# Optimization experiments

Hardware: AMD Instinct MI355X
Metric: run time of the kernel (lower is better)

## Reference

```python
import jax, jax.numpy as jnp
import numpy as np

L = 3          # num encoder layers
H = 128        # hidden_dim
NH = 8         # num_heads
HD = H // NH   # head_dim
FF = H * 4     # ff inner dim (after GLU)
B, N = 32, 512
NUM_BINS = 50


def _linear_params(key, fan_in, fan_out):
    kw, kb = jax.random.split(key)
    lim = 1.0 / np.sqrt(fan_in)
    W = jax.random.uniform(kw, (fan_in, fan_out), jnp.float32, -lim, lim)
    b = jax.random.uniform(kb, (fan_out,), jnp.float32, -lim, lim)
    return W, b


def setup_inputs() -> dict:
    key = jax.random.key(0)
    ks = jax.random.split(key, 16)
    x = jax.random.normal(ks[0], (B, N, H), jnp.float32)
    distance_matrix = jax.random.uniform(ks[1], (B, N, N), jnp.float32)
    mask = jax.random.randint(ks[2], (B, N), 0, 2).astype(bool)

    def stack_linear(k, fan_in, fan_out):
        Ws, bs = [], []
        for l in range(L):
            W, b = _linear_params(jax.random.fold_in(k, l), fan_in, fan_out)
            Ws.append(W); bs.append(b)
        return jnp.stack(Ws), jnp.stack(bs)

    Wq, bq = stack_linear(ks[3], H, H)
    Wk, bk = stack_linear(ks[4], H, H)
    Wv, bv = stack_linear(ks[5], H, H)
    Wo, bo = stack_linear(ks[6], H, H)
    dist_emb = jax.random.normal(ks[7], (L, NUM_BINS, NH), jnp.float32)
    attn_bias = jnp.zeros((L, NH, 1, 1), jnp.float32)
    g1 = jnp.ones((L, H), jnp.float32); b1 = jnp.zeros((L, H), jnp.float32)
    g2 = jnp.ones((L, H), jnp.float32); b2 = jnp.zeros((L, H), jnp.float32)
    Wf1, bf1 = stack_linear(ks[8], H, 2 * FF)
    Wf2, bf2 = stack_linear(ks[9], FF, H)
    return dict(x=x, distance_matrix=distance_matrix, mask=mask,
                Wq=Wq, bq=bq, Wk=Wk, bk=bk, Wv=Wv, bv=bv, Wo=Wo, bo=bo,
                dist_emb=dist_emb, attn_bias=attn_bias,
                g1=g1, b1=b1, g2=g2, b2=b2,
                Wf1=Wf1, bf1=bf1, Wf2=Wf2, bf2=bf2)


def _layernorm(x, g, b, eps=1e-5):
    mu = jnp.mean(x, axis=-1, keepdims=True)
    var = jnp.var(x, axis=-1, keepdims=True)
    return (x - mu) * jax.lax.rsqrt(var + eps) * g + b


def _attention(h, bins, key_mask, Wq, bq, Wk, bk, Wv, bv, Wo, bo, dist_emb, attn_bias):
    # h: [B,N,H]; bins: [B,N,N] int; key_mask: [B,N] bool (True = masked)
    Bsz, Nn, _ = h.shape
    Q = (h @ Wq + bq).reshape(Bsz, Nn, NH, HD)
    K = (h @ Wk + bk).reshape(Bsz, Nn, NH, HD)
    V = (h @ Wv + bv).reshape(Bsz, Nn, NH, HD)
    scores = jnp.einsum('bqhd,bkhd->bhqk', Q, K) / np.sqrt(HD)
    bias = jnp.transpose(dist_emb[bins], (0, 3, 1, 2))  # [B,NH,N,N]
    scores = scores + bias + attn_bias[None]
    scores = jnp.where(key_mask[:, None, None, :], -1e9, scores)
    attn = jax.nn.softmax(scores, axis=-1)
    out = jnp.einsum('bhqk,bkhd->bqhd', attn, V).reshape(Bsz, Nn, H)
    return out @ Wo + bo


def reference(x, distance_matrix, mask, Wq, bq, Wk, bk, Wv, bv, Wo, bo,
              dist_emb, attn_bias, g1, b1, g2, b2, Wf1, bf1, Wf2, bf2):
    bins = jnp.clip((distance_matrix * 10.0).astype(jnp.int32), 0, NUM_BINS - 1)
    h = x
    for l in range(L):
        # pre-LN attention block
        a = _attention(_layernorm(h, g1[l], b1[l]), bins, mask,
                       Wq[l], bq[l], Wk[l], bk[l], Wv[l], bv[l], Wo[l], bo[l],
                       dist_emb[l], attn_bias[l])
        h = h + a
        # pre-LN GLU feed-forward
        u = _layernorm(h, g2[l], b2[l]) @ Wf1[l] + bf1[l]  # [B,N,2*FF]
        ua, ub = jnp.split(u, 2, axis=-1)
        h = h + (ua * jax.nn.sigmoid(ub)) @ Wf2[l] + bf2[l]
    return h
```

## Files before the change

### kernel.cpp

```cpp
#include <hip/hip_runtime.h>
#include <stdint.h>

#define Bq 32
#define Nq 512
#define Hq 128
#define NHq 8
#define HDq 16
#define Mq (Bq * Nq)

typedef unsigned short u16;
typedef __attribute__((ext_vector_type(8))) short short8;
typedef __attribute__((ext_vector_type(8))) _Float16 half8;
typedef __attribute__((ext_vector_type(2))) __fp16 fp16x2;
typedef __attribute__((ext_vector_type(4))) float f32x4;

__device__ __forceinline__ float bf2f(u16 v) {
    return __uint_as_float(((unsigned int)v) << 16);
}
__device__ __forceinline__ float ldin(const void* p, long idx, int bf) {
    if (bf) return bf2f(((const u16*)p)[idx]);
    return ((const float*)p)[idx];
}
__device__ __forceinline__ u16 f2bf(float v) {
    unsigned int u = __float_as_uint(v);
    return (u16)((u + 0x7FFFu + ((u >> 16) & 1u)) >> 16);
}
__device__ __forceinline__ u16 f2h(float v) {
    _Float16 h = (_Float16)v;
    return *(u16*)&h;
}
__device__ __forceinline__ unsigned pk2h(float a, float b) {
    fp16x2 c = __builtin_amdgcn_cvt_pkrtz(a, b);
    return *(unsigned*)&c;
}

__global__ void prep_kernel(const void* xraw, const void* de, const void* ab,
                            const void* mraw, int* flag, float* deo, float* abo,
                            unsigned* mbits, int n) {
    __shared__ int cnt, orA, orB, orC, orD;
    int tid = threadIdx.x;
    if (tid == 0) { cnt = 0; orA = 0; orB = 0; orC = 0; orD = 0; }
    __syncthreads();
    const u16* u = (const u16*)xraw;
    int good = 0;
    for (int i = tid; i < 1024; i += 256) {
        u16 v = u[i];
        int e = (v >> 7) & 0xFF;
        if (v == 0 || (e >= 90 && e <= 141)) good++;
    }
    atomicAdd(&cnt, good);
    const uint4* p4 = (const uint4*)mraw;
    unsigned a = 0, b = 0, c = 0, d = 0;
    for (int i = tid; i < n / 16; i += 256) {
        uint4 w = p4[i];
        unsigned all = w.x | w.y | w.z | w.w;
        a |= all & 0xFEFEFEFEu;
        b |= all & 0x0000FF00u;
        c |= all & 0xFFFFFF00u;
        d |= w.y | w.w;
    }
    if (a) atomicOr(&orA, 1);
    if (b) atomicOr(&orB, 1);
    if (c) atomicOr(&orC, 1);
    if (d) atomicOr(&orD, 1);
    __syncthreads();
    int bf = (cnt >= 900);
    if (tid == 0) *flag = bf;
    int mode;
    if (orA) mode = orB ? 3 : 4;
    else if (orC) mode = 0;
    else mode = orD ? 1 : 2;
    for (int i = tid; i < 1200; i += 256) deo[i] = ldin(de, i, bf);
    if (tid < 24) abo[tid] = ldin(ab, tid, bf);
    const unsigned char* p = (const unsigned char*)mraw;
    for (int wI = tid; wI < n / 32; wI += 256) {
        unsigned word = 0;
        for (int j = 0; j < 32; ++j) {
            int i = wI * 32 + j;
            int v;
            switch (mode) {
                case 0: v = p[i]; break;
                case 1: v = ((const int*)p)[i]; break;
                case 2: v = (int)((const long long*)p)[i]; break;
                case 3: v = ((const u16*)p)[i] != 0; break;
                default: v = (((const float*)p)[i] != 0.0f); break;
            }
            if (v) word |= 1u << j;
        }
        mbits[wI] = word;
    }
}

__global__ void kprep_kernel(const unsigned* __restrict__ mbits,
                             u16* __restrict__ kidxg, int* __restrict__ nkt,
                             unsigned* __restrict__ tmask) {
    int b = blockIdx.x;
    int lane = threadIdx.x & 63;
    int pos_base = 0;
    for (int w = 0; w < 8; ++w) {
        unsigned lo = mbits[b * 16 + 2 * w], hi = mbits[b * 16 + 2 * w + 1];
        unsigned long long word = ((unsigned long long)hi << 32) | lo;
        unsigned long long un = ~word;
        int bit = (int)((un >> lane) & 1ull);
        unsigned long long before = un & ((1ull << lane) - 1ull);
        int pos = pos_base + __popcll(before);
        if (bit) kidxg[b * 512 + pos] = (u16)(w * 64 + lane);
        pos_base += __popcll(un);
    }
    int nk = pos_base;
    int nkp = (nk + 31) & ~31;
    if (nkp == 0) nkp = 32;
    int nt = nkp >> 5;
    for (int j = nk + lane; j < nkp; j += 64) kidxg[b * 512 + j] = 0;
    if (lane == 0) {
        nkt[b] = nt;
        for (int t = 0; t < 16; ++t) tmask[b * 16 + t] = 0;
        int rem = nk & 31;
        if (rem) tmask[b * 16 + nt - 1] = 0xFFFFFFFFu << rem;
        if (nk == 0) tmask[b * 16] = 0xFFFFFFFFu;
    }
}

__global__ __launch_bounds__(256) void binsc_kernel(
    const void* __restrict__ dist, const u16* __restrict__ kidxg,
    const int* __restrict__ nkt, unsigned char* __restrict__ binsc,
    const int* flagp) {
    int bf = *flagp;
    int b = blockIdx.y;
    int q0 = blockIdx.x * 8;
    __shared__ u16 kl[512];
    __shared__ int ntS;
    int tid = threadIdx.x;
    if (tid == 0) ntS = nkt[b];
    kl[tid] = kidxg[b * 512 + tid];
    kl[tid + 256] = kidxg[b * 512 + tid + 256];
    __syncthreads();
    int nkp = ntS * 32;
    for (int rq = 0; rq < 8; ++rq) {
        int q = q0 + rq;
        long rowoff = ((long)b * 512 + q) * 512;
        for (int j = tid; j < nkp; j += 256) {
            float d = ldin(dist, rowoff + kl[j], bf);
            int v = (int)(d * 10.0f);
            v = v < 0 ? 0 : (v > 49 ? 49 : v);
            binsc[((size_t)b * 512 + q) * 512 + j] = (unsigned char)(v << 2);
        }
    }
}

__global__ __launch_bounds__(256) void init_kernel(const void* x,
                                                   float* __restrict__ h,
                                                   const int* flagp) {
    int bf = *flagp;
    int i = blockIdx.x * 256 + threadIdx.x;
    long base = (long)i * 8;
    if (bf) {
        uint4 w = ((const uint4*)x)[i];
        const u16* ws = (const u16*)&w;
        float o[8];
#pragma unroll
        for (int k = 0; k < 8; ++k) o[k] = bf2f(ws[k]);
        *(float4*)&h[base] = *(float4*)&o[0];
        *(float4*)&h[base + 4] = *(float4*)&o[4];
    } else {
        float4 a = ((const float4*)x)[2 * i];
        float4 b = ((const float4*)x)[2 * i + 1];
        *(float4*)&h[base] = a;
        *(float4*)&h[base + 4] = b;
    }
}

__global__ __launch_bounds__(256) void wtrans_kernel(
    const void* Wqr, const void* Wkr, const void* Wvr, const void* Wor,
    const void* Wf1r, const void* Wf2r,
    u16* qkvT, u16* oT, u16* f1T, u16* f2T, const int* flagp) {
    int bf = *flagp;
    int bid = blockIdx.x;
    int l = bid >> 8, r = bid & 255;
    const void* src; u16* dst; long soff, doff; int Kd, Nd, t;
    if (r < 64) {
        int mat = r >> 4; t = r & 15; Kd = 128; Nd = 128;
        soff = (long)l * 16384;
        if (mat == 0)      { src = Wqr; dst = qkvT; doff = (long)l * 49152; }
        else if (mat == 1) { src = Wkr; dst = qkvT; doff = (long)l * 49152 + 16384; }
        else if (mat == 2) { src = Wvr; dst = qkvT; doff = (long)l * 49152 + 32768; }
        else               { src = Wor; dst = oT;   doff = (long)l * 16384; }
    } else if (r < 192) {
        t = r - 64; Kd = 128; Nd = 1024;
        src = Wf1r; soff = (long)l * 131072; dst = f1T; doff = (long)l * 131072;
    } else {
        t = r - 192; Kd = 512; Nd = 128;
        src = Wf2r; soff = (long)l * 65536; dst = f2T; doff = (long)l * 65536;
    }
    int ntile = Nd >> 5;
    int tk = t / ntile, tn = t % ntile;
    __shared__ u16 Ts[32][33];
    int rr = threadIdx.x >> 3, cc0 = (threadIdx.x & 7) * 4;
#pragma unroll
    for (int i = 0; i < 4; ++i) {
        long idx = soff + (long)(tk * 32 + rr) * Nd + tn * 32 + cc0 + i;
        Ts[rr][cc0 + i] = f2bf(ldin(src, idx, bf));
    }
    __syncthreads();
#pragma unroll
    for (int i = 0; i < 4; ++i) {
        long idx = doff + (long)(tn * 32 + rr) * Kd + tk * 32 + cc0 + i;
        dst[idx] = Ts[cc0 + i][rr];
    }
}

__global__ __launch_bounds__(256, 4) void qkv_mfma_kernel(
    const float* __restrict__ h, const u16* __restrict__ qkvT_l,
    const void* bqr, const void* bkr, const void* bvr, long bOff,
    const void* g1raw, const void* b1raw, long lnOff,
    u16* __restrict__ Qo, u16* __restrict__ Ko, u16* __restrict__ Vo,
    const int* flagp) {
    __shared__ __align__(16) u16 As[32][136];
    int tid = threadIdx.x;
    int m0 = blockIdx.x * 32;
    int bf = *flagp;
    {
        int row = tid >> 3, c0 = (tid & 7) * 16;
        const float* hp = h + (size_t)(m0 + row) * 128 + c0;
        float4 f0 = *(const float4*)(hp);
        float4 f1 = *(const float4*)(hp + 4);
        float4 f2 = *(const float4*)(hp + 8);
        float4 f3 = *(const float4*)(hp + 12);
        float vv[16] = {f0.x, f0.y, f0.z, f0.w, f1.x, f1.y, f1.z, f1.w,
                        f2.x, f2.y, f2.z, f2.w, f3.x, f3.y, f3.z, f3.w};
        float s = 0.f, s2 = 0.f;
#pragma unroll
        for (int k = 0; k < 16; ++k) { s += vv[k]; s2 += vv[k] * vv[k]; }
#pragma unroll
        for (int o = 1; o < 8; o <<= 1) {
            s += __shfl_xor(s, o);
            s2 += __shfl_xor(s2, o);
        }
        float mu = s * (1.0f / 128.0f);
        float var = fmaxf(s2 * (1.0f / 128.0f) - mu * mu, 0.0f);
        float rstd = rsqrtf(var + 1e-5f);
        u16 tmp[16];
#pragma unroll
        for (int k = 0; k < 16; ++k) {
            float g = ldin(g1raw, lnOff + c0 + k, bf);
            float b = ldin(b1raw, lnOff + c0 + k, bf);
            tmp[k] = f2bf((vv[k] - mu) * rstd * g + b);
        }
        *(uint4*)&As[row][c0]     = *(uint4*)&tmp[0];
        *(uint4*)&As[row][c0 + 8] = *(uint4*)&tmp[8];
    }
    __syncthreads();
    int wave = tid >> 6, lane = tid & 63;
    int q = lane >> 4, ln = lane & 15;
    int nb = wave * 32;
    f32x4 zero = {0.f, 0.f, 0.f, 0.f};
#pragma unroll
    for (int mat = 0; mat < 3; ++mat) {
        const u16* WT = qkvT_l + (size_t)mat * 16384;
        const void* braw = mat == 0 ? bqr : (mat == 1 ? bkr : bvr);
        u16* C = mat == 0 ? Qo : (mat == 1 ? Ko : Vo);
        float scale = mat == 0 ? 0.25f : 1.0f;
        short8 bfr[2][4];
#pragma unroll
        for (int t = 0; t < 2; ++t)
#pragma unroll
            for (int k4 = 0; k4 < 4; ++k4)
                bfr[t][k4] = *(const short8*)(WT + (size_t)(nb + t * 16 + ln) * 128
                                              + k4 * 32 + q * 8);
        f32x4 acc[2][2];
#pragma unroll
        for (int i = 0; i < 2; ++i)
#pragma unroll
            for (int j = 0; j < 2; ++j) acc[i][j] = zero;
#pragma unroll
        for (int k4 = 0; k4 < 4; ++k4) {
            short8 af0 = *(const short8*)&As[ln][k4 * 32 + q * 8];
            short8 af1 = *(const short8*)&As[16 + ln][k4 * 32 + q * 8];
#pragma unroll
            for (int t = 0; t < 2; ++t) {
                acc[0][t] = __builtin_amdgcn_mfma_f32_16x16x32_bf16(
                    af0, bfr[t][k4], acc[0][t], 0, 0, 0);
                acc[1][t] = __builtin_amdgcn_mfma_f32_16x16x32_bf16(
                    af1, bfr[t][k4], acc[1][t], 0, 0, 0);
            }
        }
#pragma unroll
        for (int t = 0; t < 2; ++t) {
            int n = nb + t * 16 + ln;
            float bias = ldin(braw, bOff + n, bf);
#pragma unroll
            for (int mi = 0; mi < 2; ++mi)
#pragma unroll
                for (int r = 0; r < 4; ++r) {
                    int m = m0 + mi * 16 + q * 4 + r;
                    C[(size_t)m * 128 + n] = f2h((acc[mi][t][r] + bias) * scale);
                }
        }
    }
}

__global__ __launch_bounds__(256, 3) void ffglu_kernel(
    const u16* __restrict__ att, const u16* __restrict__ oT_l,
    const void* __restrict__ bo, long boOff, float* __restrict__ h,
    const void* g2, const void* b2, long ln2Off,
    const u16* __restrict__ f1T_l, const void* __restrict__ bf1r, long bf1Off,
    const u16* __restrict__ f2T_l, const void* __restrict__ bf2r, long bf2Off,
    void* __restrict__ outp, const int* flagp) {
    __shared__ __align__(16) u16 As[32][136];
    __shared__ __align__(16) u16 vg[32][520];
    __shared__ float stats[32][4][2];
    int tid = threadIdx.x;
    int m0 = blockIdx.x * 32;
    int wave = tid >> 6, lane = tid & 63;
    int q = lane >> 4, ln = lane & 15;
    int nb = wave * 32;
    int bf = *flagp;
    f32x4 zero = {0.f, 0.f, 0.f, 0.f};

#pragma unroll
    for (int i = 0; i < 2; ++i) {
        int idx = tid + i * 256; int r = idx >> 4, c = (idx & 15) << 3;
        *(uint4*)&As[r][c] = *(const uint4*)(att + (size_t)(m0 + r) * 128 + c);
    }
    __syncthreads();
    f32x4 acc[2][2];
#pragma unroll
    for (int i = 0; i < 2; ++i)
#pragma unroll
        for (int j = 0; j < 2; ++j) acc[i][j] = zero;
    {
        short8 bfr[2][4];
#pragma unroll
        for (int t = 0; t < 2; ++t)
#pragma unroll
            for (int k4 = 0; k4 < 4; ++k4)
                bfr[t][k4] = *(const short8*)(oT_l + (size_t)(nb + t * 16 + ln) * 128
                                              + k4 * 32 + q * 8);
#pragma unroll
        for (int k4 = 0; k4 < 4; ++k4) {
            short8 af0 = *(const short8*)&As[ln][k4 * 32 + q * 8];
            short8 af1 = *(const short8*)&As[16 + ln][k4 * 32 + q * 8];
#pragma unroll
            for (int t = 0; t < 2; ++t) {
                acc[0][t] = __builtin_amdgcn_mfma_f32_16x16x32_bf16(
                    af0, bfr[t][k4], acc[0][t], 0, 0, 0);
                acc[1][t] = __builtin_amdgcn_mfma_f32_16x16x32_bf16(
                    af1, bfr[t][k4], acc[1][t], 0, 0, 0);
            }
        }
    }
    float h1[2][2][4];
    float srow[2][4], s2row[2][4];
#pragma unroll
    for (int mi = 0; mi < 2; ++mi)
#pragma unroll
        for (int r = 0; r < 4; ++r) { srow[mi][r] = 0.f; s2row[mi][r] = 0.f; }
#pragma unroll
    for (int t = 0; t < 2; ++t) {
        int n = nb + t * 16 + ln;
        float bias = ldin(bo, boOff + n, bf);
#pragma unroll
        for (int mi = 0; mi < 2; ++mi)
#pragma unroll
            for (int r = 0; r < 4; ++r) {
                float v = acc[mi][t][r] + bias +
                          h[(size_t)(m0 + mi * 16 + q * 4 + r) * 128 + n];
                h1[mi][t][r] = v;
                srow[mi][r] += v; s2row[mi][r] += v * v;
            }
    }
#pragma unroll
    for (int mi = 0; mi < 2; ++mi)
#pragma unroll
        for (int r = 0; r < 4; ++r)
#pragma unroll
            for (int o = 1; o < 16; o <<= 1) {
                srow[mi][r] += __shfl_xor(srow[mi][r], o);
                s2row[mi][r] += __shfl_xor(s2row[mi][r], o);
            }
    if (ln == 0) {
#pragma unroll
        for (int mi = 0; mi < 2; ++mi)
#pragma unroll
            for (int r = 0; r < 4; ++r) {
                stats[mi * 16 + q * 4 + r][wave][0] = srow[mi][r];
                stats[mi * 16 + q * 4 + r][wave][1] = s2row[mi][r];
            }
    }
    __syncthreads();
    float mu[2][4], rs[2][4];
#pragma unroll
    for (int mi = 0; mi < 2; ++mi)
#pragma unroll
        for (int r = 0; r < 4; ++r) {
            int row = mi * 16 + q * 4 + r;
            float s = (stats[row][0][0] + stats[row][1][0]) +
                      (stats[row][2][0] + stats[row][3][0]);
            float s2 = (stats[row][0][1] + stats[row][1][1]) +
                       (stats[row][2][1] + stats[row][3][1]);
            mu[mi][r] = s * (1.0f / 128.0f);
            float var = fmaxf(s2 * (1.0f / 128.0f) - mu[mi][r] * mu[mi][r], 0.0f);
            rs[mi][r] = rsqrtf(var + 1e-5f);
        }
#pragma unroll
    for (int t = 0; t < 2; ++t) {
        int n = nb + t * 16 + ln;
        float g = ldin(g2, ln2Off + n, bf), bb = ldin(b2, ln2Off + n, bf);
#pragma unroll
        for (int mi = 0; mi < 2; ++mi)
#pragma unroll
            for (int r = 0; r < 4; ++r)
                As[mi * 16 + q * 4 + r][n] =
                    f2bf((h1[mi][t][r] - mu[mi][r]) * rs[mi][r] * g + bb);
    }
    __syncthreads();
    int nb16 = wave * 16;
    for (int ch = 0; ch < 8; ++ch) {
        int arow = ch * 64 + nb16;
        short8 ba[4], bb8[4];
#pragma unroll
        for (int k4 = 0; k4 < 4; ++k4) {
            ba[k4]  = *(const short8*)(f1T_l + (size_t)(arow + ln) * 128
                                       + k4 * 32 + q * 8);
            bb8[k4] = *(const short8*)(f1T_l + (size_t)(512 + arow + ln) * 128
                                       + k4 * 32 + q * 8);
        }
        f32x4 aA[2] = {zero, zero}, aB[2] = {zero, zero};
#pragma unroll
        for (int k4 = 0; k4 < 4; ++k4) {
            short8 af0 = *(const short8*)&As[ln][k4 * 32 + q * 8];
            short8 af1 = *(const short8*)&As[16 + ln][k4 * 32 + q * 8];
            aA[0] = __builtin_amdgcn_mfma_f32_16x16x32_bf16(af0, ba[k4], aA[0], 0, 0, 0);
            aA[1] = __builtin_amdgcn_mfma_f32_16x16x32_bf16(af1, ba[k4], aA[1], 0, 0, 0);
            aB[0] = __builtin_amdgcn_mfma_f32_16x16x32_bf16(af0, bb8[k4], aB[0], 0, 0, 0);
            aB[1] = __builtin_amdgcn_mfma_f32_16x16x32_bf16(af1, bb8[k4], aB[1], 0, 0, 0);
        }
        int n = arow + ln;
        float bA = ldin(bf1r, bf1Off + n, bf);
        float bB = ldin(bf1r, bf1Off + 512 + n, bf);
#pragma unroll
        for (int mi = 0; mi < 2; ++mi)
#pragma unroll
            for (int r = 0; r < 4; ++r) {
                float ua = aA[mi][r] + bA, ub = aB[mi][r] + bB;
                vg[mi * 16 + q * 4 + r][n] = f2bf(ua / (1.0f + __expf(-ub)));
            }
    }
    __syncthreads();
    f32x4 accF[2][2];
#pragma unroll
    for (int i = 0; i < 2; ++i)
#pragma unroll
        for (int j = 0; j < 2; ++j) accF[i][j] = zero;
    for (int fc = 0; fc < 4; ++fc) {
        short8 bfr[2][4];
#pragma unroll
        for (int t = 0; t < 2; ++t)
#pragma unroll
            for (int k4 = 0; k4 < 4; ++k4)
                bfr[t][k4] = *(const short8*)(f2T_l + (size_t)(nb + t * 16 + ln) * 512
                                              + fc * 128 + k4 * 32 + q * 8);
#pragma unroll
        for (int k4 = 0; k4 < 4; ++k4) {
            short8 af0 = *(const short8*)&vg[ln][fc * 128 + k4 * 32 + q * 8];
            short8 af1 = *(const short8*)&vg[16 + ln][fc * 128 + k4 * 32 + q * 8];
#pragma unroll
            for (int t = 0; t < 2; ++t) {
                accF[0][t] = __builtin_amdgcn_mfma_f32_16x16x32_bf16(
                    af0, bfr[t][k4], accF[0][t], 0, 0, 0);
                accF[1][t] = __builtin_amdgcn_mfma_f32_16x16x32_bf16(
                    af1, bfr[t][k4], accF[1][t], 0, 0, 0);
            }
        }
    }
#pragma unroll
    for (int t = 0; t < 2; ++t) {
        int n = nb + t * 16 + ln;
        float bias = ldin(bf2r, bf2Off + n, bf);
#pragma unroll
        for (int mi = 0; mi < 2; ++mi)
#pragma unroll
            for (int r = 0; r < 4; ++r) {
                int m = m0 + mi * 16 + q * 4 + r;
                float v = accF[mi][t][r] + bias + h1[mi][t][r];
                h[(size_t)m * 128 + n] = v;
                if (outp) {
                    if (bf) ((u16*)outp)[(size_t)m * 128 + n] = f2bf(v);
                    else ((float*)outp)[(size_t)m * 128 + n] = v;
                }
            }
    }
}

__global__ __launch_bounds__(256, 4) void attn_kernel(
    const u16* __restrict__ Qh, const u16* __restrict__ Kh,
    const u16* __restrict__ Vh, const unsigned char* __restrict__ binsc,
    const u16* __restrict__ kidxg, const int* __restrict__ nktp,
    const unsigned* __restrict__ tmaskp, const float* __restrict__ deL,
    const float* __restrict__ abL, u16* __restrict__ out) {
    int id = blockIdx.x;
    int c = id & 7, t5 = id >> 3;
    int nh = t5 & 7;
    int pair = ((t5 >> 3) << 3) | c;
    int b = pair >> 2, qq = pair & 3;

    __shared__ __align__(16) u16 KsF[8192];
    __shared__ __align__(16) u16 VT[16 * 520];
    __shared__ __align__(16) u16 Pl[4 * 16 * 40];

    int tid = threadIdx.x;
    int nt = __builtin_amdgcn_readfirstlane(nktp[b]);
    int nkp = nt * 32;
    const u16* Kp = Kh + (size_t)(b * Nq) * Hq + nh * HDq;
    const u16* Vp = Vh + (size_t)(b * Nq) * Hq + nh * HDq;
    for (int r = tid; r < nkp; r += 256) {
        int row = kidxg[b * 512 + r];
        int kt = r >> 5, s = (r >> 4) & 1, lnr = r & 15;
        uint4 k0v = *(const uint4*)(Kp + (size_t)row * Hq);
        uint4 k1v = *(const uint4*)(Kp + (size_t)row * Hq + 8);
        *(uint4*)&KsF[kt * 512 + s * 256 + lnr * 8]       = k0v;
        *(uint4*)&KsF[kt * 512 + s * 256 + 128 + lnr * 8] = k1v;
        uint4 v0 = *(const uint4*)(Vp + (size_t)row * Hq);
        uint4 v1 = *(const uint4*)(Vp + (size_t)row * Hq + 8);
        u16 vv[16];
        *(uint4*)&vv[0] = v0; *(uint4*)&vv[8] = v1;
#pragma unroll
        for (int d = 0; d < 16; ++d) VT[d * 520 + r] = vv[d];
    }
    __syncthreads();

    int wave = tid >> 6, lane = tid & 63;
    int quad = lane >> 4, ln = lane & 15;
    int q0w = qq * 128 + wave * 32;

    float tblf = (lane < 50) ? deL[lane * NHq + nh] + abL[nh] : 0.0f;
    int tbli = __float_as_int(tblf);
    unsigned tl = tmaskp[b * 16 + nt - 1];

    half8 qf[2];
#pragma unroll
    for (int t = 0; t < 2; ++t) {
        uint4 qv = {0, 0, 0, 0};
        if (quad < 2)
            qv = *(const uint4*)(Qh + (size_t)(b * Nq + q0w + t * 16 + ln) * Hq
                                 + nh * HDq + quad * 8);
        qf[t] = *(half8*)&qv;
    }

    f32x4 zero = {0.f, 0.f, 0.f, 0.f};
    f32x4 acc[2] = {zero, zero};
    float zp[2] = {0.f, 0.f};
    _Float16* Pw = (_Float16*)&Pl[wave * 640];
    const _Float16* KsH = (const _Float16*)KsF;
    const _Float16* VTH = (const _Float16*)VT;
    const unsigned char* brow0 = binsc + ((size_t)b * 512 + (q0w + ln)) * 512;
    const unsigned char* brow1 = brow0 + (size_t)16 * 512;

    unsigned pb00 = *(const unsigned*)(brow0 + quad * 4);
    unsigned pb01 = *(const unsigned*)(brow0 + 16 + quad * 4);
    unsigned pb10 = *(const unsigned*)(brow1 + quad * 4);
    unsigned pb11 = *(const unsigned*)(brow1 + 16 + quad * 4);

    for (int kt = 0; kt < nt; ++kt) {
        int k0 = kt * 32;
        unsigned w = (kt == nt - 1) ? tl : 0u;
        unsigned cb00 = pb00, cb01 = pb01, cb10 = pb10, cb11 = pb11;
        if (kt < nt - 1) {
            pb00 = *(const unsigned*)(brow0 + k0 + 32 + quad * 4);
            pb01 = *(const unsigned*)(brow0 + k0 + 48 + quad * 4);
            pb10 = *(const unsigned*)(brow1 + k0 + 32 + quad * 4);
            pb11 = *(const unsigned*)(brow1 + k0 + 48 + quad * 4);
        }
        half8 vb = *(const half8*)(VTH + ln * 520 + k0 + quad * 8);
        half8 ka0 = {}, ka1 = {};
        if (quad < 2) {
            ka0 = *(const half8*)(KsH + kt * 512 + quad * 128 + ln * 8);
            ka1 = *(const half8*)(KsH + kt * 512 + 256 + quad * 128 + ln * 8);
        }
#pragma unroll
        for (int t = 0; t < 2; ++t) {
            unsigned bw0 = t == 0 ? cb00 : cb10;
            unsigned bw1 = t == 0 ? cb01 : cb11;
            f32x4 s0 = __builtin_amdgcn_mfma_f32_16x16x32_f16(ka0, qf[t], zero, 0, 0, 0);
            f32x4 s1 = __builtin_amdgcn_mfma_f32_16x16x32_f16(ka1, qf[t], zero, 0, 0, 0);
            float p[8];
#pragma unroll
            for (int r = 0; r < 4; ++r) {
                float bias = __int_as_float(__builtin_amdgcn_ds_bpermute(
                    (int)((bw0 >> (8 * r)) & 0xFFu), tbli));
                float sc = s0[r] + bias;
                bool m = (w >> (quad * 4 + r)) & 1u;
                p[r] = m ? 0.0f : __expf(sc);
            }
#pragma unroll
            for (int r = 0; r < 4; ++r) {
                float bias = __int_as_float(__builtin_amdgcn_ds_bpermute(
                    (int)((bw1 >> (8 * r)) & 0xFFu), tbli));
                float sc = s1[r] + bias;
                bool m = (w >> (16 + quad * 4 + r)) & 1u;
                p[4 + r] = m ? 0.0f : __expf(sc);
            }
            zp[t] += ((p[0] + p[1]) + (p[2] + p[3])) +
                     ((p[4] + p[5]) + (p[6] + p[7]));
            uint2 w0, w1;
            w0.x = pk2h(p[0], p[1]); w0.y = pk2h(p[2], p[3]);
            w1.x = pk2h(p[4], p[5]); w1.y = pk2h(p[6], p[7]);
            *(uint2*)(Pw + ln * 40 + quad * 4)      = w0;
            *(uint2*)(Pw + ln * 40 + 16 + quad * 4) = w1;
            half8 pa = *(const half8*)(Pw + ln * 40 + quad * 8);
            acc[t] = __builtin_amdgcn_mfma_f32_16x16x32_f16(pa, vb, acc[t], 0, 0, 0);
        }
    }
#pragma unroll
    for (int t = 0; t < 2; ++t) {
        zp[t] += __shfl_xor(zp[t], 16);
        zp[t] += __shfl_xor(zp[t], 32);
    }
#pragma unroll
    for (int t = 0; t < 2; ++t) {
#pragma unroll
        for (int r = 0; r < 4; ++r) {
            float zz = __shfl(zp[t], quad * 4 + r);
            float val = acc[t][r] / fmaxf(zz, 1e-35f);
            int qrow = q0w + t * 16 + quad * 4 + r;
            out[(size_t)(b * Nq + qrow) * Hq + nh * HDq + ln] = f2bf(val);
        }
    }
}

extern "C" void kernel_launch(void* const* d_in, const int* in_sizes, int n_in,
                              void* d_out, int out_size, void* d_ws, size_t ws_size,
                              hipStream_t stream) {
    const void* x  = d_in[0];
    const void* dist = d_in[1];
    const void* mask = d_in[2];
    const void* Wq = d_in[3];  const void* bq = d_in[4];
    const void* Wk = d_in[5];  const void* bk = d_in[6];
    const void* Wv = d_in[7];  const void* bv = d_in[8];
    const void* Wo = d_in[9];  const void* bo = d_in[10];
    const void* de = d_in[11]; const void* ab = d_in[12];
    const void* g1 = d_in[13]; const void* b1 = d_in[14];
    const void* g2 = d_in[15]; const void* b2 = d_in[16];
    const void* Wf1 = d_in[17]; const void* bf1 = d_in[18];
    const void* Wf2 = d_in[19]; const void* bf2 = d_in[20];

    char* ws = (char*)d_ws;
    const size_t OFF_DE   = 64;
    const size_t OFF_AB   = 5120;
    const size_t OFF_BINS = 8192;
    const size_t OFF_MSK  = OFF_BINS + 8388608;
    const size_t OFF_KIDX = OFF_MSK + 4096;
    const size_t OFF_NKT  = OFF_KIDX + 32768;
    const size_t OFF_TM   = OFF_NKT + 256;
    const size_t OFF_H    = OFF_TM + 4096;
    const size_t OFF_QKV  = OFF_H + 8388608;
    const size_t OFF_ATT  = OFF_QKV + 25165824;
    const size_t OFF_WT   = OFF_ATT + 4194304;
    const size_t NEEDED   = OFF_WT + 1572864;
    if (ws_size < NEEDED) return;

    int* flag = (int*)ws;
    float* deF = (float*)(ws + OFF_DE);
    float* abF = (float*)(ws + OFF_AB);
    unsigned char* binsc = (unsigned char*)(ws + OFF_BINS);
    unsigned* mbits = (unsigned*)(ws + OFF_MSK);
    u16* kidxg = (u16*)(ws + OFF_KIDX);
    int* nkt = (int*)(ws + OFF_NKT);
    unsigned* tmask = (unsigned*)(ws + OFF_TM);
    float* h = (float*)(ws + OFF_H);
    u16* Qh = (u16*)(ws + OFF_QKV);
    u16* Kh = Qh + 2097152;
    u16* Vh = Qh + 2 * 2097152;
    u16* att = (u16*)(ws + OFF_ATT);
    u16* qkvT = (u16*)(ws + OFF_WT);
    u16* oT  = qkvT + 147456;
    u16* f1T = oT + 49152;
    u16* f2T = f1T + 393216;

    prep_kernel<<<1, 256, 0, stream>>>(x, de, ab, mask, flag, deF, abF, mbits, Bq * Nq);
    kprep_kernel<<<32, 64, 0, stream>>>(mbits, kidxg, nkt, tmask);
    dim3 gbc(64, 32);
    binsc_kernel<<<gbc, 256, 0, stream>>>(dist, kidxg, nkt, binsc, flag);
    init_kernel<<<1024, 256, 0, stream>>>(x, h, flag);
    wtrans_kernel<<<768, 256, 0, stream>>>(Wq, Wk, Wv, Wo, Wf1, Wf2,
                                           qkvT, oT, f1T, f2T, flag);

    for (int l = 0; l < 3; ++l) {
        qkv_mfma_kernel<<<512, 256, 0, stream>>>(h, qkvT + (size_t)l * 49152,
                                                 bq, bk, bv, (long)l * Hq,
                                                 g1, b1, (long)l * Hq,
                                                 Qh, Kh, Vh, flag);
        attn_kernel<<<1024, 256, 0, stream>>>(Qh, Kh, Vh, binsc, kidxg, nkt, tmask,
                                              deF + (long)l * 400, abF + (long)l * 8, att);
        ffglu_kernel<<<512, 256, 0, stream>>>(
            att, oT + (size_t)l * 16384, bo, (long)l * Hq,
            h, g2, b2, (long)l * Hq,
            f1T + (size_t)l * 131072, bf1, (long)l * 1024,
            f2T + (size_t)l * 65536, bf2, (long)l * Hq,
            l == 2 ? d_out : nullptr, flag);
    }
}
```

Before: 371.7 us.

## Fuse setup kernels and fold next-layer QKV projection into FFN kernel

Merges the mask-index preparation into the single-block prep kernel, and combines bin computation, input conversion and weight transposition into one launch split by block index. The FFN/GLU kernel now also runs the next layer's LayerNorm and QKV MFMA projection on its freshly produced 32-row tile, so the separate per-layer QKV launches for layers 1 and 2 go away. This removes several launches and a round trip of h through global memory, but it raises register and shared-memory pressure in the FFN kernel and puts the 32-batch index scan into one block.

```diff
diff --git a/kernel.cpp b/kernel.cpp
--- a/kernel.cpp
+++ b/kernel.cpp
@@ -36,8 +36,11 @@
 
 __global__ void prep_kernel(const void* xraw, const void* de, const void* ab,
                             const void* mraw, int* flag, float* deo, float* abo,
-                            unsigned* mbits, int n) {
+                            unsigned* mbits, int n,
+                            u16* __restrict__ kidxg, int* __restrict__ nkt,
+                            unsigned* __restrict__ tmask) {
     __shared__ int cnt, orA, orB, orC, orD;
+    __shared__ unsigned smb[512];
     int tid = threadIdx.x;
     if (tid == 0) { cnt = 0; orA = 0; orB = 0; orC = 0; orD = 0; }
     __syncthreads();
@@ -88,124 +91,117 @@
             if (v) word |= 1u << j;
         }
         mbits[wI] = word;
-    }
-}
-
-__global__ void kprep_kernel(const unsigned* __restrict__ mbits,
-                             u16* __restrict__ kidxg, int* __restrict__ nkt,
-                             unsigned* __restrict__ tmask) {
-    int b = blockIdx.x;
-    int lane = threadIdx.x & 63;
-    int pos_base = 0;
-    for (int w = 0; w < 8; ++w) {
-        unsigned lo = mbits[b * 16 + 2 * w], hi = mbits[b * 16 + 2 * w + 1];
-        unsigned long long word = ((unsigned long long)hi << 32) | lo;
-        unsigned long long un = ~word;
-        int bit = (int)((un >> lane) & 1ull);
-        unsigned long long before = un & ((1ull << lane) - 1ull);
-        int pos = pos_base + __popcll(before);
-        if (bit) kidxg[b * 512 + pos] = (u16)(w * 64 + lane);
-        pos_base += __popcll(un);
-    }
-    int nk = pos_base;
-    int nkp = (nk + 31) & ~31;
-    if (nkp == 0) nkp = 32;
-    int nt = nkp >> 5;
-    for (int j = nk + lane; j < nkp; j += 64) kidxg[b * 512 + j] = 0;
-    if (lane == 0) {
-        nkt[b] = nt;
-        for (int t = 0; t < 16; ++t) tmask[b * 16 + t] = 0;
-        int rem = nk & 31;
-        if (rem) tmask[b * 16 + nt - 1] = 0xFFFFFFFFu << rem;
-        if (nk == 0) tmask[b * 16] = 0xFFFFFFFFu;
-    }
-}
-
-__global__ __launch_bounds__(256) void binsc_kernel(
+        smb[wI] = word;
+    }
+    __syncthreads();
+    int lane = tid & 63;
+    for (int bb = tid >> 6; bb < 32; bb += 4) {
+        int pos_base = 0;
+        for (int w = 0; w < 8; ++w) {
+            unsigned lo = smb[bb * 16 + 2 * w], hi = smb[bb * 16 + 2 * w + 1];
+            unsigned long long word = ((unsigned long long)hi << 32) | lo;
+            unsigned long long un = ~word;
+            int bit = (int)((un >> lane) & 1ull);
+            unsigned long long before = un & ((1ull << lane) - 1ull);
+            int pos = pos_base + __popcll(before);
+            if (bit) kidxg[bb * 512 + pos] = (u16)(w * 64 + lane);
+            pos_base += __popcll(un);
+        }
+        int nk = pos_base;
+        int nkp = (nk + 31) & ~31;
+        if (nkp == 0) nkp = 32;
+        int nt = nkp >> 5;
+        for (int j = nk + lane; j < nkp; j += 64) kidxg[bb * 512 + j] = 0;
+        if (lane == 0) {
+            nkt[bb] = nt;
+            for (int t = 0; t < 16; ++t) tmask[bb * 16 + t] = 0;
+            int rem = nk & 31;
+            if (rem) tmask[bb * 16 + nt - 1] = 0xFFFFFFFFu << rem;
+            if (nk == 0) tmask[bb * 16] = 0xFFFFFFFFu;
+        }
+    }
+}
+
+__global__ __launch_bounds__(256) void setup2_kernel(
     const void* __restrict__ dist, const u16* __restrict__ kidxg,
-    const int* __restrict__ nkt, unsigned char* __restrict__ binsc,
-    const int* flagp) {
-    int bf = *flagp;
-    int b = blockIdx.y;
-    int q0 = blockIdx.x * 8;
-    __shared__ u16 kl[512];
-    __shared__ int ntS;
-    int tid = threadIdx.x;
-    if (tid == 0) ntS = nkt[b];
-    kl[tid] = kidxg[b * 512 + tid];
-    kl[tid + 256] = kidxg[b * 512 + tid + 256];
-    __syncthreads();
-    int nkp = ntS * 32;
-    for (int rq = 0; rq < 8; ++rq) {
-        int q = q0 + rq;
-        long rowoff = ((long)b * 512 + q) * 512;
-        for (int j = tid; j < nkp; j += 256) {
-            float d = ldin(dist, rowoff + kl[j], bf);
-            int v = (int)(d * 10.0f);
-            v = v < 0 ? 0 : (v > 49 ? 49 : v);
-            binsc[((size_t)b * 512 + q) * 512 + j] = (unsigned char)(v << 2);
-        }
-    }
-}
-
-__global__ __launch_bounds__(256) void init_kernel(const void* x,
-                                                   float* __restrict__ h,
-                                                   const int* flagp) {
-    int bf = *flagp;
-    int i = blockIdx.x * 256 + threadIdx.x;
-    long base = (long)i * 8;
-    if (bf) {
-        uint4 w = ((const uint4*)x)[i];
-        const u16* ws = (const u16*)&w;
-        float o[8];
-#pragma unroll
-        for (int k = 0; k < 8; ++k) o[k] = bf2f(ws[k]);
-        *(float4*)&h[base] = *(float4*)&o[0];
-        *(float4*)&h[base + 4] = *(float4*)&o[4];
-    } else {
-        float4 a = ((const float4*)x)[2 * i];
-        float4 b = ((const float4*)x)[2 * i + 1];
-        *(float4*)&h[base] = a;
-        *(float4*)&h[base + 4] = b;
-    }
-}
-
-__global__ __launch_bounds__(256) void wtrans_kernel(
+    const int* __restrict__ nktp, unsigned char* __restrict__ binsc,
+    const void* x, float* __restrict__ h,
     const void* Wqr, const void* Wkr, const void* Wvr, const void* Wor,
     const void* Wf1r, const void* Wf2r,
     u16* qkvT, u16* oT, u16* f1T, u16* f2T, const int* flagp) {
+    __shared__ u16 kl[512];
+    __shared__ int ntS;
+    __shared__ u16 Ts[32][33];
+    int id = blockIdx.x;
+    int tid = threadIdx.x;
     int bf = *flagp;
-    int bid = blockIdx.x;
-    int l = bid >> 8, r = bid & 255;
-    const void* src; u16* dst; long soff, doff; int Kd, Nd, t;
-    if (r < 64) {
-        int mat = r >> 4; t = r & 15; Kd = 128; Nd = 128;
-        soff = (long)l * 16384;
-        if (mat == 0)      { src = Wqr; dst = qkvT; doff = (long)l * 49152; }
-        else if (mat == 1) { src = Wkr; dst = qkvT; doff = (long)l * 49152 + 16384; }
-        else if (mat == 2) { src = Wvr; dst = qkvT; doff = (long)l * 49152 + 32768; }
-        else               { src = Wor; dst = oT;   doff = (long)l * 16384; }
-    } else if (r < 192) {
-        t = r - 64; Kd = 128; Nd = 1024;
-        src = Wf1r; soff = (long)l * 131072; dst = f1T; doff = (long)l * 131072;
+    if (id < 2048) {
+        int b = id >> 6;
+        int q0 = (id & 63) * 8;
+        if (tid == 0) ntS = nktp[b];
+        kl[tid] = kidxg[b * 512 + tid];
+        kl[tid + 256] = kidxg[b * 512 + tid + 256];
+        __syncthreads();
+        int nkp = ntS * 32;
+        for (int rq = 0; rq < 8; ++rq) {
+            int q = q0 + rq;
+            long rowoff = ((long)b * 512 + q) * 512;
+            for (int j = tid; j < nkp; j += 256) {
+                float d = ldin(dist, rowoff + kl[j], bf);
+                int v = (int)(d * 10.0f);
+                v = v < 0 ? 0 : (v > 49 ? 49 : v);
+                binsc[((size_t)b * 512 + q) * 512 + j] = (unsigned char)(v << 2);
+            }
+        }
+    } else if (id < 3072) {
+        int i = (id - 2048) * 256 + tid;
+        long base = (long)i * 8;
+        if (bf) {
+            uint4 w = ((const uint4*)x)[i];
+            const u16* ws = (const u16*)&w;
+            float o[8];
+#pragma unroll
+            for (int k = 0; k < 8; ++k) o[k] = bf2f(ws[k]);
+            *(float4*)&h[base] = *(float4*)&o[0];
+            *(float4*)&h[base + 4] = *(float4*)&o[4];
+        } else {
+            float4 a = ((const float4*)x)[2 * i];
+            float4 b2v = ((const float4*)x)[2 * i + 1];
+            *(float4*)&h[base] = a;
+            *(float4*)&h[base + 4] = b2v;
+        }
     } else {
-        t = r - 192; Kd = 512; Nd = 128;
-        src = Wf2r; soff = (long)l * 65536; dst = f2T; doff = (long)l * 65536;
-    }
-    int ntile = Nd >> 5;
-    int tk = t / ntile, tn = t % ntile;
-    __shared__ u16 Ts[32][33];
-    int rr = threadIdx.x >> 3, cc0 = (threadIdx.x & 7) * 4;
-#pragma unroll
-    for (int i = 0; i < 4; ++i) {
-        long idx = soff + (long)(tk * 32 + rr) * Nd + tn * 32 + cc0 + i;
-        Ts[rr][cc0 + i] = f2bf(ldin(src, idx, bf));
-    }
-    __syncthreads();
-#pragma unroll
-    for (int i = 0; i < 4; ++i) {
-        long idx = doff + (long)(tn * 32 + rr) * Kd + tk * 32 + cc0 + i;
-        dst[idx] = Ts[cc0 + i][rr];
+        int bid = id - 3072;
+        int l = bid >> 8, r = bid & 255;
+        const void* src; u16* dst; long soff, doff; int Kd, Nd, t;
+        if (r < 64) {
+            int mat = r >> 4; t = r & 15; Kd = 128; Nd = 128;
+            soff = (long)l * 16384;
+            if (mat == 0)      { src = Wqr; dst = qkvT; doff = (long)l * 49152; }
+            else if (mat == 1) { src = Wkr; dst = qkvT; doff = (long)l * 49152 + 16384; }
+            else if (mat == 2) { src = Wvr; dst = qkvT; doff = (long)l * 49152 + 32768; }
+            else               { src = Wor; dst = oT;   doff = (long)l * 16384; }
+        } else if (r < 192) {
+            t = r - 64; Kd = 128; Nd = 1024;
+            src = Wf1r; soff = (long)l * 131072; dst = f1T; doff = (long)l * 131072;
+        } else {
+            t = r - 192; Kd = 512; Nd = 128;
+            src = Wf2r; soff = (long)l * 65536; dst = f2T; doff = (long)l * 65536;
+        }
+        int ntile = Nd >> 5;
+        int tk = t / ntile, tn = t % ntile;
+        int rr = tid >> 3, cc0 = (tid & 7) * 4;
+#pragma unroll
+        for (int i = 0; i < 4; ++i) {
+            long idx = soff + (long)(tk * 32 + rr) * Nd + tn * 32 + cc0 + i;
+            Ts[rr][cc0 + i] = f2bf(ldin(src, idx, bf));
+        }
+        __syncthreads();
+#pragma unroll
+        for (int i = 0; i < 4; ++i) {
+            long idx = doff + (long)(tn * 32 + rr) * Kd + tk * 32 + cc0 + i;
+            dst[idx] = Ts[cc0 + i][rr];
+        }
     }
 }
 
@@ -305,7 +301,11 @@
     const void* g2, const void* b2, long ln2Off,
     const u16* __restrict__ f1T_l, const void* __restrict__ bf1r, long bf1Off,
     const u16* __restrict__ f2T_l, const void* __restrict__ bf2r, long bf2Off,
-    void* __restrict__ outp, const int* flagp) {
+    void* __restrict__ outp, const int* flagp,
+    const u16* __restrict__ qkvTn,
+    const void* bqr, const void* bkr, const void* bvr, long bOffN,
+    const void* g1, const void* b1, long ln1OffN,
+    u16* __restrict__ Qo, u16* __restrict__ Ko, u16* __restrict__ Vo) {
     __shared__ __align__(16) u16 As[32][136];
     __shared__ __align__(16) u16 vg[32][520];
     __shared__ float stats[32][4][2];
@@ -484,11 +484,113 @@
                 int m = m0 + mi * 16 + q * 4 + r;
                 float v = accF[mi][t][r] + bias + h1[mi][t][r];
                 h[(size_t)m * 128 + n] = v;
+                h1[mi][t][r] = v;
                 if (outp) {
                     if (bf) ((u16*)outp)[(size_t)m * 128 + n] = f2bf(v);
                     else ((float*)outp)[(size_t)m * 128 + n] = v;
                 }
             }
+    }
+    if (!qkvTn) return;
+#pragma unroll
+    for (int mi = 0; mi < 2; ++mi)
+#pragma unroll
+        for (int r = 0; r < 4; ++r) { srow[mi][r] = 0.f; s2row[mi][r] = 0.f; }
+#pragma unroll
+    for (int t = 0; t < 2; ++t)
+#pragma unroll
+        for (int mi = 0; mi < 2; ++mi)
+#pragma unroll
+            for (int r = 0; r < 4; ++r) {
+                float v = h1[mi][t][r];
+                srow[mi][r] += v; s2row[mi][r] += v * v;
+            }
+#pragma unroll
+    for (int mi = 0; mi < 2; ++mi)
+#pragma unroll
+        for (int r = 0; r < 4; ++r)
+#pragma unroll
+            for (int o = 1; o < 16; o <<= 1) {
+                srow[mi][r] += __shfl_xor(srow[mi][r], o);
+                s2row[mi][r] += __shfl_xor(s2row[mi][r], o);
+            }
+    if (ln == 0) {
+#pragma unroll
+        for (int mi = 0; mi < 2; ++mi)
+#pragma unroll
+            for (int r = 0; r < 4; ++r) {
+                stats[mi * 16 + q * 4 + r][wave][0] = srow[mi][r];
+                stats[mi * 16 + q * 4 + r][wave][1] = s2row[mi][r];
+            }
+    }
+    __syncthreads();
+#pragma unroll
+    for (int mi = 0; mi < 2; ++mi)
+#pragma unroll
+        for (int r = 0; r < 4; ++r) {
+            int row = mi * 16 + q * 4 + r;
+            float s = (stats[row][0][0] + stats[row][1][0]) +
+                      (stats[row][2][0] + stats[row][3][0]);
+            float s2 = (stats[row][0][1] + stats[row][1][1]) +
+                       (stats[row][2][1] + stats[row][3][1]);
+            mu[mi][r] = s * (1.0f / 128.0f);
+            float var = fmaxf(s2 * (1.0f / 128.0f) - mu[mi][r] * mu[mi][r], 0.0f);
+            rs[mi][r] = rsqrtf(var + 1e-5f);
+        }
+#pragma unroll
+    for (int t = 0; t < 2; ++t) {
+        int n = nb + t * 16 + ln;
+        float g = ldin(g1, ln1OffN + n, bf), bb = ldin(b1, ln1OffN + n, bf);
+#pragma unroll
+        for (int mi = 0; mi < 2; ++mi)
+#pragma unroll
+            for (int r = 0; r < 4; ++r)
+                As[mi * 16 + q * 4 + r][n] =
+                    f2bf((h1[mi][t][r] - mu[mi][r]) * rs[mi][r] * g + bb);
+    }
+    __syncthreads();
+#pragma unroll
+    for (int mat = 0; mat < 3; ++mat) {
+        const u16* WT = qkvTn + (size_t)mat * 16384;
+        const void* braw = mat == 0 ? bqr : (mat == 1 ? bkr : bvr);
+        u16* C = mat == 0 ? Qo : (mat == 1 ? Ko : Vo);
+        float scale = mat == 0 ? 0.25f : 1.0f;
+        short8 bfr[2][4];
+#pragma unroll
+        for (int t = 0; t < 2; ++t)
+#pragma unroll
+            for (int k4 = 0; k4 < 4; ++k4)
+                bfr[t][k4] = *(const short8*)(WT + (size_t)(nb + t * 16 + ln) * 128
+                                              + k4 * 32 + q * 8);
+        f32x4 aq[2][2];
+#pragma unroll
+        for (int i = 0; i < 2; ++i)
+#pragma unroll
+            for (int j = 0; j < 2; ++j) aq[i][j] = zero;
+#pragma unroll
+        for (int k4 = 0; k4 < 4; ++k4) {
+            short8 af0 = *(const short8*)&As[ln][k4 * 32 + q * 8];
+            short8 af1 = *(const short8*)&As[16 + ln][k4 * 32 + q * 8];
+#pragma unroll
+            for (int t = 0; t < 2; ++t) {
+                aq[0][t] = __builtin_amdgcn_mfma_f32_16x16x32_bf16(
+                    af0, bfr[t][k4], aq[0][t], 0, 0, 0);
+                aq[1][t] = __builtin_amdgcn_mfma_f32_16x16x32_bf16(
+                    af1, bfr[t][k4], aq[1][t], 0, 0, 0);
+            }
+        }
+#pragma unroll
+        for (int t = 0; t < 2; ++t) {
+            int n = nb + t * 16 + ln;
+            float bias = ldin(braw, bOffN + n, bf);
+#pragma unroll
+            for (int mi = 0; mi < 2; ++mi)
+#pragma unroll
+                for (int r = 0; r < 4; ++r) {
+                    int m = m0 + mi * 16 + q * 4 + r;
+                    C[(size_t)m * 128 + n] = f2h((aq[mi][t][r] + bias) * scale);
+                }
+        }
     }
 }
 
@@ -677,19 +779,14 @@
     u16* f1T = oT + 49152;
     u16* f2T = f1T + 393216;
 
-    prep_kernel<<<1, 256, 0, stream>>>(x, de, ab, mask, flag, deF, abF, mbits, Bq * Nq);
-    kprep_kernel<<<32, 64, 0, stream>>>(mbits, kidxg, nkt, tmask);
-    dim3 gbc(64, 32);
-    binsc_kernel<<<gbc, 256, 0, stream>>>(dist, kidxg, nkt, binsc, flag);
-    init_kernel<<<1024, 256, 0, stream>>>(x, h, flag);
-    wtrans_kernel<<<768, 256, 0, stream>>>(Wq, Wk, Wv, Wo, Wf1, Wf2,
-                                           qkvT, oT, f1T, f2T, flag);
-
+    prep_kernel<<<1, 256, 0, stream>>>(x, de, ab, mask, flag, deF, abF, mbits,
+                                       Bq * Nq, kidxg, nkt, tmask);
+    setup2_kernel<<<3840, 256, 0, stream>>>(dist, kidxg, nkt, binsc, x, h,
+                                            Wq, Wk, Wv, Wo, Wf1, Wf2,
+                                            qkvT, oT, f1T, f2T, flag);
+    qkv_mfma_kernel<<<512, 256, 0, stream>>>(h, qkvT, bq, bk, bv, 0,
+                                             g1, b1, 0, Qh, Kh, Vh, flag);
     for (int l = 0; l < 3; ++l) {
-        qkv_mfma_kernel<<<512, 256, 0, stream>>>(h, qkvT + (size_t)l * 49152,
-                                                 bq, bk, bv, (long)l * Hq,
-                                                 g1, b1, (long)l * Hq,
-                                                 Qh, Kh, Vh, flag);
         attn_kernel<<<1024, 256, 0, stream>>>(Qh, Kh, Vh, binsc, kidxg, nkt, tmask,
                                               deF + (long)l * 400, abF + (long)l * 8, att);
         ffglu_kernel<<<512, 256, 0, stream>>>(
@@ -697,6 +794,10 @@
             h, g2, b2, (long)l * Hq,
             f1T + (size_t)l * 131072, bf1, (long)l * 1024,
             f2T + (size_t)l * 65536, bf2, (long)l * Hq,
-            l == 2 ? d_out : nullptr, flag);
-    }
-}
+            l == 2 ? d_out : nullptr, flag,
+            l < 2 ? qkvT + (size_t)(l + 1) * 49152 : (const u16*)nullptr,
+            bq, bk, bv, (long)(l + 1) * Hq,
+            g1, b1, (long)(l + 1) * Hq,
+            Qh, Kh, Vh);
+    }
+}
```

Result: faster. 355.2 us (-4.4%).
